# Performance work log

Measured on AMD Instinct MI355X. Metric: run time of the kernel, lower is better.

Reference implementation:

```python
import jax, jax.numpy as jnp
import numpy as np

N = 50000      # nodes
E = 800000     # edges
H = 128        # hidden_features
DEPTH = 5
G = 64         # graphs in batch
EPS = 1e-5


def _ln(x, g, b):
    m = jnp.mean(x, axis=-1, keepdims=True)
    v = jnp.mean((x - m) ** 2, axis=-1, keepdims=True)
    return (x - m) * jax.lax.rsqrt(v + EPS) * g + b


def _lin_init(key, fan_in, fan_out):
    s = 1.0 / np.sqrt(fan_in)
    kw, kb = jax.random.split(key)
    return (jax.random.uniform(kw, (fan_in, fan_out), jnp.float32, -s, s),
            jax.random.uniform(kb, (fan_out,), jnp.float32, -s, s))


def setup_inputs() -> dict:
    key = jax.random.key(0)
    ks = jax.random.split(key, 16)
    inp = {
        'x': jax.random.normal(ks[0], (N, 1), jnp.float32),
        'pos': jax.random.normal(ks[1], (N, 3), jnp.float32),
        'edge_index': jax.random.randint(ks[2], (2, E), 0, N, jnp.int32),
        'cell_offset': jax.random.normal(ks[3], (E, 3), jnp.float32),
        'unit_cell': jax.random.normal(ks[4], (3, 3), jnp.float32),
        'batch_ids': jnp.sort(jax.random.randint(ks[5], (N,), 0, G, jnp.int32)),
    }
    inp['emb_w'], inp['emb_b'] = _lin_init(ks[6], 1, H)
    # stacked per-layer params for lax.scan
    def stack(fn):
        outs = [fn(jax.random.fold_in(ks[7], i)) for i in range(DEPTH)]
        return tuple(jnp.stack(t) for t in zip(*outs))
    def layer_params(k):
        k1, k2, k3, k4 = jax.random.split(k, 4)
        mw1, mb1 = _lin_init(k1, 2 * H + 1, H)
        mw2, mb2 = _lin_init(k2, H, H)
        uw1, ub1 = _lin_init(k3, 2 * H, H)
        uw2, ub2 = _lin_init(k4, H, H)
        ones = jnp.ones((H,), jnp.float32); zeros = jnp.zeros((H,), jnp.float32)
        return (mw1, mb1, ones, zeros, mw2, mb2, ones, zeros,
                uw1, ub1, ones, zeros, uw2, ub2, ones, zeros)
    (inp['msg_w1'], inp['msg_b1'], inp['msg_g1'], inp['msg_be1'],
     inp['msg_w2'], inp['msg_b2'], inp['msg_g2'], inp['msg_be2'],
     inp['upd_w1'], inp['upd_b1'], inp['upd_g1'], inp['upd_be1'],
     inp['upd_w2'], inp['upd_b2'], inp['upd_g2'], inp['upd_be2']) = stack(layer_params)
    inp['pred_w1'], inp['pred_b1'] = _lin_init(ks[8], H, H)
    inp['pred_w2'], inp['pred_b2'] = _lin_init(ks[9], H, 1)
    return inp


def reference(x, pos, edge_index, cell_offset, unit_cell, batch_ids,
              emb_w, emb_b,
              msg_w1, msg_b1, msg_g1, msg_be1, msg_w2, msg_b2, msg_g2, msg_be2,
              upd_w1, upd_b1, upd_g1, upd_be1, upd_w2, upd_b2, upd_g2, upd_be2,
              pred_w1, pred_b1, pred_w2, pred_b2):
    src, dst = edge_index[0], edge_index[1]  # PyG: x_j = source, x_i = target
    h = x @ emb_w + emb_b  # [N, H]
    # PBC distances
    corrected = pos[dst] - cell_offset @ unit_cell  # [E, 3]
    dist = jnp.linalg.norm(corrected - pos[src], axis=-1, keepdims=True)  # [E, 1]

    def step(h, p):
        (mw1, mb1, mg1, mbe1, mw2, mb2, mg2, mbe2,
         uw1, ub1, ug1, ube1, uw2, ub2, ug2, ube2) = p
        msg = jnp.concatenate([h[dst], h[src], dist], axis=-1)  # [E, 2H+1]
        msg = jax.nn.relu(_ln(msg @ mw1 + mb1, mg1, mbe1))
        msg = jax.nn.relu(_ln(msg @ mw2 + mb2, mg2, mbe2))
        aggr = jax.ops.segment_sum(msg, dst, num_segments=N)  # scatter-add to targets
        u = jnp.concatenate([h, aggr], axis=-1)  # [N, 2H]
        u = jax.nn.relu(_ln(u @ uw1 + ub1, ug1, ube1))
        u = jax.nn.relu(_ln(u @ uw2 + ub2, ug2, ube2))
        return h + u, None  # residual

    params = (msg_w1, msg_b1, msg_g1, msg_be1, msg_w2, msg_b2, msg_g2, msg_be2,
              upd_w1, upd_b1, upd_g1, upd_be1, upd_w2, upd_b2, upd_g2, upd_be2)
    h, _ = jax.lax.scan(step, h, params)
    pooled = jax.ops.segment_sum(h, batch_ids, num_segments=G)  # global_add_pool
    return jax.nn.relu(pooled @ pred_w1 + pred_b1) @ pred_w2 + pred_b2  # [G, 1]
```

## Files before the change

kernel.cpp:

```cpp
#include <hip/hip_runtime.h>
#include <hip/hip_bf16.h>

#define NN 50000
#define NE 800000
#define HD 128
#define DEPTH 5
#define NG 64
#define LNEPS 1e-5f

typedef __attribute__((ext_vector_type(8))) short bf8;
typedef __attribute__((ext_vector_type(4))) float f4;

static __device__ __forceinline__ unsigned short bf1(float x) {
    __hip_bfloat16 b = __float2bfloat16(x);
    unsigned short r;
    __builtin_memcpy(&r, &b, 2);
    return r;
}
static __device__ __forceinline__ unsigned int cvt2(float a, float b) {
    float2 t; t.x = a; t.y = b;
    __hip_bfloat162 h = __float22bfloat162_rn(t);
    unsigned int r;
    __builtin_memcpy(&r, &h, 4);
    return r;
}


__global__ void pack_weights(const float* __restrict__ msg_w1, const float* __restrict__ msg_w2,
                             const float* __restrict__ upd_w1, const float* __restrict__ upd_w2,
                             unsigned short* __restrict__ packed) {
    const int which = blockIdx.y & 3, layer = blockIdx.y >> 2;
    const int t = blockIdx.x * 256 + threadIdx.x;
    unsigned short* lbase = packed + layer * 98304;
    if (which == 0) {
        if (t >= 32768) return;
        const int e = t & 7, l = (t >> 3) & 63, f = (t >> 9) & 15, s = t >> 13;
        const int k = s*32 + ((l >> 4) << 3) + e;
        const float* W = msg_w1 + layer*257*HD;
        const float v = (f < 8) ? W[k*HD + f*16 + (l & 15)]
                                : W[(k + 128)*HD + (f - 8)*16 + (l & 15)];
        lbase[t] = bf1(v);
        return;
    }
    const float* src; int K; unsigned short* dst;
    if (which == 1)      { src = msg_w2 + layer*HD*HD;  K = 128; dst = lbase + 32768; }
    else if (which == 2) { src = upd_w1 + layer*256*HD; K = 256; dst = lbase + 49152; }
    else                 { src = upd_w2 + layer*HD*HD;  K = 128; dst = lbase + 81920; }
    if (t >= K * HD) return;
    const int e = t & 7, l = (t >> 3) & 63, f = (t >> 9) & 7, s = t >> 12;
    const int kk = s*32 + ((l >> 4) << 3) + e;
    const int k = (which & 1) ? ((kk & 7)*16 + (kk >> 3)) : kk;
    const int n = f*16 + (l & 15);
    dst[t] = bf1(src[k*HD + n]);
}

__global__ void pack_sig(const float* __restrict__ msg_w1, const float* __restrict__ msg_g1,
                         const float* __restrict__ msg_be1, float* __restrict__ sig) {
    const int t = blockIdx.x * 256 + threadIdx.x;
    if (t >= DEPTH * 384) return;
    const int layer = t / 384, w3 = (t % 384) / 128, i = t % 128;
    const int col = (i & 7)*16 + (i >> 3);
    float v;
    if (w3 == 0)      v = msg_w1[layer*257*HD + 256*HD + col];
    else if (w3 == 1) v = msg_g1[layer*HD + col];
    else              v = msg_be1[layer*HD + col];
    sig[t] = v;
}

__global__ void embed_kernel(const float* __restrict__ x, const float* __restrict__ emb_w,
                             const float* __restrict__ emb_b,
                             float* __restrict__ h, unsigned short* __restrict__ hb) {
    const int i = blockIdx.x * 256 + threadIdx.x;
    const int n = i >> 7, j = i & 127;
    const float v = x[n] * emb_w[j] + emb_b[j];
    h[i] = v; hb[i] = bf1(v);
}

__global__ void hist_kernel(const int* __restrict__ ei, int* __restrict__ cnt) {
    const int e = blockIdx.x * 256 + threadIdx.x;
    atomicAdd(&cnt[ei[NE + e]], 1);
}

__global__ __launch_bounds__(1024) void scan_kernel(const int* __restrict__ cnt,
                                                    int* __restrict__ cur) {
    __shared__ int part[1024];
    const int t = threadIdx.x;
    const int per = 49;
    const int base = t * per;
    int s = 0;
    for (int i = 0; i < per; ++i) { const int idx = base + i; if (idx < NN) s += cnt[idx]; }
    part[t] = s; __syncthreads();
    for (int st = 1; st < 1024; st <<= 1) {
        const int v = (t >= st) ? part[t - st] : 0;
        __syncthreads();
        part[t] += v;
        __syncthreads();
    }
    int run = (t == 0) ? 0 : part[t - 1];
    for (int i = 0; i < per; ++i) {
        const int idx = base + i;
        if (idx < NN) { cur[idx] = run; run += cnt[idx]; }
    }
}

__global__ void scatter_kernel(const int* __restrict__ ei, int* __restrict__ cur,
                               int* __restrict__ sidx, int* __restrict__ ssrc,
                               int* __restrict__ sdst) {
    const int e = blockIdx.x * 256 + threadIdx.x;
    const int d = ei[NE + e];
    const int p = atomicAdd(&cur[d], 1);
    sidx[p] = e; ssrc[p] = ei[e]; sdst[p] = d;
}

__global__ void dist_kernel(const float* __restrict__ pos, const int* __restrict__ sidx,
                            const int* __restrict__ ssrc, const int* __restrict__ sdst,
                            const float* __restrict__ cell, const float* __restrict__ U,
                            float* __restrict__ dist) {
    const int p = blockIdx.x * 256 + threadIdx.x;
    const int e = sidx[p];
    const int s = ssrc[p], d = sdst[p];
    const float c0 = cell[e*3], c1 = cell[e*3+1], c2 = cell[e*3+2];
    const float ox = c0*U[0] + c1*U[3] + c2*U[6];
    const float oy = c0*U[1] + c1*U[4] + c2*U[7];
    const float oz = c0*U[2] + c1*U[5] + c2*U[8];
    const float dx = pos[d*3]   - ox - pos[s*3];
    const float dy = pos[d*3+1] - oy - pos[s*3+1];
    const float dz = pos[d*3+2] - oz - pos[s*3+2];
    dist[p] = sqrtf(dx*dx + dy*dy + dz*dz);
}

__global__ void y_kernel(const unsigned short* __restrict__ hb,
                         const unsigned short* __restrict__ pw,
                         const float* __restrict__ b1, unsigned short* __restrict__ y) {
    const int tid = threadIdx.x, blk = blockIdx.x;
    const int l = tid & 63, wv = tid >> 6;
    const int li = l & 15, gq = l >> 4;
    const int rowA = wv*32 + li, rowB = rowA + 16;
    const int nA = blk*64 + rowA, nB = blk*64 + rowB;
    const int ncA = (nA < NN) ? nA : NN - 1;
    const int ncB = (nB < NN) ? nB : NN - 1;
    const unsigned short* pHA = hb + ncA*HD + gq*8;
    const unsigned short* pHB = hb + ncB*HD + gq*8;

    f4 acc[2][16];
    #pragma unroll
    for (int m = 0; m < 2; ++m)
        #pragma unroll
        for (int f = 0; f < 16; ++f) { f4 z = {0.f,0.f,0.f,0.f}; acc[m][f] = z; }

    #pragma unroll
    for (int s = 0; s < 4; ++s) {
        const bf8 aA = *(const bf8*)(pHA + s*32);
        const bf8 aB = *(const bf8*)(pHB + s*32);
        #pragma unroll
        for (int f = 0; f < 16; ++f) {
            const bf8 b = *(const bf8*)(pw + s*8192 + f*512 + l*8);
            acc[0][f] = __builtin_amdgcn_mfma_f32_16x16x32_bf16(aA, b, acc[0][f], 0, 0, 0);
            acc[1][f] = __builtin_amdgcn_mfma_f32_16x16x32_bf16(aB, b, acc[1][f], 0, 0, 0);
        }
    }

    float bv[8];
    #pragma unroll
    for (int f = 0; f < 8; ++f) bv[f] = b1[f*16 + li];

    #pragma unroll
    for (int m = 0; m < 2; ++m)
        #pragma unroll
        for (int r = 0; r < 4; ++r) {
            const int node = blk*64 + wv*32 + m*16 + gq*4 + r;
            if (node < NN) {
                uint4 u;
                u.x = cvt2(acc[m][0][r]+bv[0], acc[m][1][r]+bv[1]);
                u.y = cvt2(acc[m][2][r]+bv[2], acc[m][3][r]+bv[3]);
                u.z = cvt2(acc[m][4][r]+bv[4], acc[m][5][r]+bv[5]);
                u.w = cvt2(acc[m][6][r]+bv[6], acc[m][7][r]+bv[7]);
                *(uint4*)(y + node*256 + li*8) = u;
                uint4 v;
                v.x = cvt2(acc[m][8][r],  acc[m][9][r]);
                v.y = cvt2(acc[m][10][r], acc[m][11][r]);
                v.z = cvt2(acc[m][12][r], acc[m][13][r]);
                v.w = cvt2(acc[m][14][r], acc[m][15][r]);
                *(uint4*)(y + node*256 + 128 + li*8) = v;
            }
        }
}

__global__ __launch_bounds__(128, 4) void edge_kernel(
    const unsigned short* __restrict__ y, const float* __restrict__ dist,
    const int* __restrict__ ssrc, const int* __restrict__ sdst,
    const unsigned short* __restrict__ pw2, const float* __restrict__ sig,
    const float* __restrict__ b2, const float* __restrict__ g2,
    const float* __restrict__ be2, float* __restrict__ aggr)
{
    __shared__ unsigned short lds[64 * 128];
    __shared__ int dstl[64];
    char* ldsb = (char*)lds;
    const int tid = threadIdx.x, blk = blockIdx.x;
    const int l = tid & 63, wv = tid >> 6;
    const int li = l & 15, gq = l >> 4;

    if (tid < 64) dstl[tid] = sdst[blk*64 + tid];

    {
        const int rl = l >> 1, half = l & 1;
        const int row = wv*32 + rl;
        const int e = blk*64 + row;
        const int dn = sdst[e], sn = ssrc[e];
        const float dv = dist[e];
        const unsigned short* pd = y + dn*256 + half*64;
        const unsigned short* pS = y + sn*256 + 128 + half*64;
        const float* wl = sig + half*64;

        float msum[64];
        #pragma unroll
        for (int c = 0; c < 8; ++c) {
            const uint4 ud = *(const uint4*)(pd + c*8);
            const uint4 us = *(const uint4*)(pS + c*8);
            const float4 wa = *(const float4*)(wl + c*8);
            const float4 wb = *(const float4*)(wl + c*8 + 4);
            const unsigned int du[4] = {ud.x, ud.y, ud.z, ud.w};
            const unsigned int su[4] = {us.x, us.y, us.z, us.w};
            const float ww[8] = {wa.x,wa.y,wa.z,wa.w, wb.x,wb.y,wb.z,wb.w};
            #pragma unroll
            for (int k = 0; k < 4; ++k) {
                const float d0 = __uint_as_float(du[k] << 16);
                const float d1 = __uint_as_float(du[k] & 0xffff0000u);
                const float s0 = __uint_as_float(su[k] << 16);
                const float s1 = __uint_as_float(su[k] & 0xffff0000u);
                msum[c*8 + 2*k]     = d0 + s0 + dv*ww[2*k];
                msum[c*8 + 2*k + 1] = d1 + s1 + dv*ww[2*k+1];
            }
        }
        float s1 = 0.f, s2 = 0.f;
        #pragma unroll
        for (int i = 0; i < 64; ++i) { s1 += msum[i]; s2 += msum[i]*msum[i]; }
        s1 += __shfl_xor(s1, 1);
        s2 += __shfl_xor(s2, 1);
        const float mean = s1 * (1.f/HD);
        const float rstd = rsqrtf(s2*(1.f/HD) - mean*mean + LNEPS);

        const float* g1p = sig + 128 + half*64;
        const float* e1p = sig + 256 + half*64;
        const int rsw = (row & 7) << 4;
        const int base = row*256 + half*128;
        #pragma unroll
        for (int c = 0; c < 8; ++c) {
            const float4 ga = *(const float4*)(g1p + c*8);
            const float4 gb = *(const float4*)(g1p + c*8 + 4);
            const float4 ea = *(const float4*)(e1p + c*8);
            const float4 eb = *(const float4*)(e1p + c*8 + 4);
            const float gg[8] = {ga.x,ga.y,ga.z,ga.w, gb.x,gb.y,gb.z,gb.w};
            const float ee[8] = {ea.x,ea.y,ea.z,ea.w, eb.x,eb.y,eb.z,eb.w};
            float t[8];
            #pragma unroll
            for (int k = 0; k < 8; ++k)
                t[k] = fmaxf((msum[c*8+k] - mean)*rstd*gg[k] + ee[k], 0.f);
            uint4 u;
            u.x = cvt2(t[0], t[1]); u.y = cvt2(t[2], t[3]);
            u.z = cvt2(t[4], t[5]); u.w = cvt2(t[6], t[7]);
            *(uint4*)(ldsb + ((base + c*16) ^ rsw)) = u;
        }
    }

    f4 acc2[2][8];
    #pragma unroll
    for (int m = 0; m < 2; ++m)
        #pragma unroll
        for (int f = 0; f < 8; ++f) { f4 z = {0.f,0.f,0.f,0.f}; acc2[m][f] = z; }
    #pragma unroll
    for (int s = 0; s < 4; ++s) {
        bf8 breg[8];
        #pragma unroll
        for (int f = 0; f < 8; ++f) breg[f] = *(const bf8*)(pw2 + s*4096 + f*512 + l*8);
        #pragma unroll
        for (int m = 0; m < 2; ++m) {
            const int ar = wv*32 + m*16 + li;
            const bf8 a = *(const bf8*)(ldsb + ((ar*256 + s*64 + gq*16) ^ ((ar & 7) << 4)));
            #pragma unroll
            for (int f = 0; f < 8; ++f)
                acc2[m][f] = __builtin_amdgcn_mfma_f32_16x16x32_bf16(a, breg[f], acc2[m][f], 0, 0, 0);
        }
    }

    {
        float bb2[8], gg2[8], be2v[8];
        #pragma unroll
        for (int f = 0; f < 8; ++f) {
            const int n = f*16 + li;
            bb2[f] = b2[n]; gg2[f] = g2[n]; be2v[f] = be2[n];
        }
        #pragma unroll
        for (int m = 0; m < 2; ++m) {
            float ps[4] = {0,0,0,0}, pq[4] = {0,0,0,0};
            #pragma unroll
            for (int f = 0; f < 8; ++f)
                #pragma unroll
                for (int r = 0; r < 4; ++r) {
                    const float v = acc2[m][f][r] + bb2[f];
                    acc2[m][f][r] = v;
                    ps[r] += v; pq[r] += v*v;
                }
            #pragma unroll
            for (int mm = 1; mm < 16; mm <<= 1)
                #pragma unroll
                for (int r = 0; r < 4; ++r) {
                    ps[r] += __shfl_xor(ps[r], mm);
                    pq[r] += __shfl_xor(pq[r], mm);
                }
            #pragma unroll
            for (int r = 0; r < 4; ++r) {
                const float mean = ps[r] * (1.f/HD);
                const float rstd = rsqrtf(pq[r]*(1.f/HD) - mean*mean + LNEPS);
                const int row = wv*32 + m*16 + gq*4 + r;
                float vv[8];
                #pragma unroll
                for (int f = 0; f < 8; ++f)
                    vv[f] = fmaxf((acc2[m][f][r] - mean)*rstd*gg2[f] + be2v[f], 0.f);
                uint4 u;
                u.x = cvt2(vv[0], vv[1]); u.y = cvt2(vv[2], vv[3]);
                u.z = cvt2(vv[4], vv[5]); u.w = cvt2(vv[6], vv[7]);
                *(uint4*)(ldsb + ((row*256 + li*16) ^ ((row & 7) << 4))) = u;
            }
        }
    }
    __syncthreads();

    {
        const int j = tid;
        const int jj = (j & 7)*16 + (j >> 3);
        int curd = dstl[0];
        float a0 = 0.f;
        #pragma unroll 4
        for (int row = 0; row < 64; ++row) {
            const int d = dstl[row];
            const unsigned short u = *(const unsigned short*)(ldsb + ((row*256 + j*2) ^ ((row & 7) << 4)));
            const float v = __uint_as_float(((unsigned int)u) << 16);
            if (d != curd) { unsafeAtomicAdd(&aggr[curd*HD + jj], a0); a0 = 0.f; curd = d; }
            a0 += v;
        }
        unsafeAtomicAdd(&aggr[curd*HD + jj], a0);
    }
}

__global__ __launch_bounds__(128, 4) void node_kernel(
    unsigned short* __restrict__ hb, float* __restrict__ aggr,
    const unsigned short* __restrict__ pw,
    const float* __restrict__ b1, const float* __restrict__ g1, const float* __restrict__ be1,
    const float* __restrict__ b2, const float* __restrict__ g2, const float* __restrict__ be2,
    float* __restrict__ h)
{
    __shared__ unsigned short lds[64 * 128];
    char* ldsb = (char*)lds;
    const int tid = threadIdx.x, blk = blockIdx.x;
    const int l = tid & 63, wv = tid >> 6;
    const int li = l & 15, gq = l >> 4;

    const int rowA = wv*32 + li, rowB = rowA + 16;
    const int nA = blk*64 + rowA, nB = blk*64 + rowB;
    const int ncA = (nA < NN) ? nA : NN - 1;
    const int ncB = (nB < NN) ? nB : NN - 1;
    const unsigned short* pHA = hb + ncA*HD + gq*8;
    const unsigned short* pHB = hb + ncB*HD + gq*8;
    float* pAA = aggr + ncA*HD + gq*8;
    float* pAB = aggr + ncB*HD + gq*8;

    f4 acc[2][8];
    #pragma unroll
    for (int m = 0; m < 2; ++m)
        #pragma unroll
        for (int f = 0; f < 8; ++f) { f4 z = {0.f,0.f,0.f,0.f}; acc[m][f] = z; }

    #pragma unroll
    for (int s = 0; s < 8; ++s) {
        bf8 breg[8];
        #pragma unroll
        for (int f = 0; f < 8; ++f) breg[f] = *(const bf8*)(pw + s*4096 + f*512 + l*8);
        bf8 aA, aB;
        if (s < 4) {
            aA = *(const bf8*)(pHA + s*32);
            aB = *(const bf8*)(pHB + s*32);
        } else {
            const float4 a0 = *(const float4*)(pAA + (s-4)*32);
            const float4 a1 = *(const float4*)(pAA + (s-4)*32 + 4);
            const float4 c0 = *(const float4*)(pAB + (s-4)*32);
            const float4 c1 = *(const float4*)(pAB + (s-4)*32 + 4);
            union { unsigned int u[4]; bf8 v; } pk;
            pk.u[0] = cvt2(a0.x, a0.y); pk.u[1] = cvt2(a0.z, a0.w);
            pk.u[2] = cvt2(a1.x, a1.y); pk.u[3] = cvt2(a1.z, a1.w);
            aA = pk.v;
            pk.u[0] = cvt2(c0.x, c0.y); pk.u[1] = cvt2(c0.z, c0.w);
            pk.u[2] = cvt2(c1.x, c1.y); pk.u[3] = cvt2(c1.z, c1.w);
            aB = pk.v;
        }
        #pragma unroll
        for (int f = 0; f < 8; ++f) {
            acc[0][f] = __builtin_amdgcn_mfma_f32_16x16x32_bf16(aA, breg[f], acc[0][f], 0, 0, 0);
            acc[1][f] = __builtin_amdgcn_mfma_f32_16x16x32_bf16(aB, breg[f], acc[1][f], 0, 0, 0);
        }
    }

    {
        const float4 z = {0.f,0.f,0.f,0.f};
        #pragma unroll
        for (int s = 0; s < 4; ++s) {
            if (nA < NN) { *(float4*)(pAA + s*32) = z; *(float4*)(pAA + s*32 + 4) = z; }
            if (nB < NN) { *(float4*)(pAB + s*32) = z; *(float4*)(pAB + s*32 + 4) = z; }
        }
    }

    {
        float bb[8], gg[8], be[8];
        #pragma unroll
        for (int f = 0; f < 8; ++f) {
            const int n = f*16 + li;
            bb[f] = b1[n]; gg[f] = g1[n]; be[f] = be1[n];
        }
        #pragma unroll
        for (int m = 0; m < 2; ++m) {
            float ps[4] = {0,0,0,0}, pq[4] = {0,0,0,0};
            #pragma unroll
            for (int f = 0; f < 8; ++f)
                #pragma unroll
                for (int r = 0; r < 4; ++r) {
                    const float v = acc[m][f][r] + bb[f];
                    acc[m][f][r] = v;
                    ps[r] += v; pq[r] += v*v;
                }
            #pragma unroll
            for (int mm = 1; mm < 16; mm <<= 1)
                #pragma unroll
                for (int r = 0; r < 4; ++r) {
                    ps[r] += __shfl_xor(ps[r], mm);
                    pq[r] += __shfl_xor(pq[r], mm);
                }
            #pragma unroll
            for (int r = 0; r < 4; ++r) {
                const float mean = ps[r] * (1.f/HD);
                const float rstd = rsqrtf(pq[r]*(1.f/HD) - mean*mean + LNEPS);
                const int row = wv*32 + m*16 + gq*4 + r;
                float vv[8];
                #pragma unroll
                for (int f = 0; f < 8; ++f)
                    vv[f] = fmaxf((acc[m][f][r] - mean)*rstd*gg[f] + be[f], 0.f);
                uint4 u;
                u.x = cvt2(vv[0], vv[1]); u.y = cvt2(vv[2], vv[3]);
                u.z = cvt2(vv[4], vv[5]); u.w = cvt2(vv[6], vv[7]);
                *(uint4*)(ldsb + ((row*256 + li*16) ^ ((row & 7) << 4))) = u;
            }
        }
    }

    const unsigned short* pw2 = pw + 32768;
    f4 acc2[2][8];
    #pragma unroll
    for (int m = 0; m < 2; ++m)
        #pragma unroll
        for (int f = 0; f < 8; ++f) { f4 z = {0.f,0.f,0.f,0.f}; acc2[m][f] = z; }
    #pragma unroll
    for (int s = 0; s < 4; ++s) {
        bf8 breg[8];
        #pragma unroll
        for (int f = 0; f < 8; ++f) breg[f] = *(const bf8*)(pw2 + s*4096 + f*512 + l*8);
        #pragma unroll
        for (int m = 0; m < 2; ++m) {
            const int ar = wv*32 + m*16 + li;
            const bf8 a = *(const bf8*)(ldsb + ((ar*256 + s*64 + gq*16) ^ ((ar & 7) << 4)));
            #pragma unroll
            for (int f = 0; f < 8; ++f)
                acc2[m][f] = __builtin_amdgcn_mfma_f32_16x16x32_bf16(a, breg[f], acc2[m][f], 0, 0, 0);
        }
    }

    {
        float bb2[8], gg2[8], be2v[8];
        #pragma unroll
        for (int f = 0; f < 8; ++f) {
            const int n = f*16 + li;
            bb2[f] = b2[n]; gg2[f] = g2[n]; be2v[f] = be2[n];
        }
        #pragma unroll
        for (int m = 0; m < 2; ++m) {
            float ps[4] = {0,0,0,0}, pq[4] = {0,0,0,0};
            #pragma unroll
            for (int f = 0; f < 8; ++f)
                #pragma unroll
                for (int r = 0; r < 4; ++r) {
                    const float v = acc2[m][f][r] + bb2[f];
                    acc2[m][f][r] = v;
                    ps[r] += v; pq[r] += v*v;
                }
            #pragma unroll
            for (int mm = 1; mm < 16; mm <<= 1)
                #pragma unroll
                for (int r = 0; r < 4; ++r) {
                    ps[r] += __shfl_xor(ps[r], mm);
                    pq[r] += __shfl_xor(pq[r], mm);
                }
            #pragma unroll
            for (int r = 0; r < 4; ++r) {
                const int node = blk*64 + wv*32 + m*16 + gq*4 + r;
                if (node < NN) {
                    const float mean = ps[r] * (1.f/HD);
                    const float rstd = rsqrtf(pq[r]*(1.f/HD) - mean*mean + LNEPS);
                    #pragma unroll
                    for (int f = 0; f < 8; ++f) {
                        const int n = f*16 + li;
                        float v = (acc2[m][f][r] - mean)*rstd*gg2[f] + be2v[f];
                        v = fmaxf(v, 0.f);
                        const int idx = node*HD + n;
                        const float nh = h[idx] + v;
                        h[idx] = nh;
                        hb[idx] = bf1(nh);
                    }
                }
            }
        }
    }
}

__global__ void pool_kernel(const float* __restrict__ h, const int* __restrict__ bids,
                            float* __restrict__ pooled) {
    const int j = threadIdx.x;
    const int n0 = blockIdx.x * 256;
    if (n0 >= NN) return;
    int cur = bids[n0];
    float acc = 0.f;
    for (int i = 0; i < 256; ++i) {
        const int n = n0 + i;
        if (n >= NN) break;
        const int b = bids[n];
        if (b != cur) { unsafeAtomicAdd(&pooled[cur*HD + j], acc); acc = 0.f; cur = b; }
        acc += h[n*HD + j];
    }
    unsafeAtomicAdd(&pooled[cur*HD + j], acc);
}

__global__ void pred_kernel(const float* __restrict__ pooled, const float* __restrict__ w1,
                            const float* __restrict__ pb1, const float* __restrict__ w2,
                            const float* __restrict__ pb2, float* __restrict__ out) {
    const int g = blockIdx.x, j = threadIdx.x;
    __shared__ float pg[128];
    __shared__ float red[128];
    pg[j] = pooled[g*HD + j];
    __syncthreads();
    float z = pb1[j];
    for (int k = 0; k < 128; ++k) z += pg[k] * w1[k*HD + j];
    red[j] = fmaxf(z, 0.f) * w2[j];
    __syncthreads();
    for (int st = 64; st > 0; st >>= 1) {
        if (j < st) red[j] += red[j + st];
        __syncthreads();
    }
    if (j == 0) out[g] = red[0] + pb2[0];
}

extern "C" void kernel_launch(void* const* d_in, const int* in_sizes, int n_in,
                              void* d_out, int out_size, void* d_ws, size_t ws_size,
                              hipStream_t stream) {
    const float* x       = (const float*)d_in[0];
    const float* pos     = (const float*)d_in[1];
    const int*   ei      = (const int*)  d_in[2];
    const float* cell    = (const float*)d_in[3];
    const float* U       = (const float*)d_in[4];
    const int*   bids    = (const int*)  d_in[5];
    const float* emb_w   = (const float*)d_in[6];
    const float* emb_b   = (const float*)d_in[7];
    const float* msg_w1  = (const float*)d_in[8];
    const float* msg_b1  = (const float*)d_in[9];
    const float* msg_g1  = (const float*)d_in[10];
    const float* msg_be1 = (const float*)d_in[11];
    const float* msg_w2  = (const float*)d_in[12];
    const float* msg_b2  = (const float*)d_in[13];
    const float* msg_g2  = (const float*)d_in[14];
    const float* msg_be2 = (const float*)d_in[15];
    const float* upd_w1  = (const float*)d_in[16];
    const float* upd_b1  = (const float*)d_in[17];
    const float* upd_g1  = (const float*)d_in[18];
    const float* upd_be1 = (const float*)d_in[19];
    const float* upd_w2  = (const float*)d_in[20];
    const float* upd_b2  = (const float*)d_in[21];
    const float* upd_g2  = (const float*)d_in[22];
    const float* upd_be2 = (const float*)d_in[23];
    const float* pred_w1 = (const float*)d_in[24];
    const float* pred_b1 = (const float*)d_in[25];
    const float* pred_w2 = (const float*)d_in[26];
    const float* pred_b2 = (const float*)d_in[27];

    char* ws = (char*)d_ws;
    float*          h      = (float*)          ws;
    unsigned short* hb     = (unsigned short*)(ws + 25600000);
    float*          aggr   = (float*)         (ws + 38400000);
    float*          dist   = (float*)         (ws + 64000000);
    float*          pooled = (float*)         (ws + 67200000);
    unsigned short* packed = (unsigned short*)(ws + 67232768);
    int*            cnt    = (int*)           (ws + 68215808);
    int*            cur    = (int*)           (ws + 68416512);
    int*            sidx   = (int*)           (ws + 68617216);
    int*            ssrc   = (int*)           (ws + 71817216);
    int*            sdst   = (int*)           (ws + 75017216);
    float*          sig    = (float*)         (ws + 78217216);
    unsigned short* y      = (unsigned short*)(ws + 78224896);

    hipMemsetAsync(aggr, 0, (size_t)NN * HD * sizeof(float), stream);
    hipMemsetAsync(pooled, 0, (size_t)NG * HD * sizeof(float), stream);
    hipMemsetAsync(cnt, 0, (size_t)NN * sizeof(int), stream);

    dim3 pgrid(128, DEPTH * 4);
    pack_weights<<<pgrid, 256, 0, stream>>>(msg_w1, msg_w2, upd_w1, upd_w2, packed);
    pack_sig<<<(DEPTH*384 + 255)/256, 256, 0, stream>>>(msg_w1, msg_g1, msg_be1, sig);
    embed_kernel<<<(NN * HD) / 256, 256, 0, stream>>>(x, emb_w, emb_b, h, hb);

    hist_kernel<<<NE / 256, 256, 0, stream>>>(ei, cnt);
    scan_kernel<<<1, 1024, 0, stream>>>(cnt, cur);
    scatter_kernel<<<NE / 256, 256, 0, stream>>>(ei, cur, sidx, ssrc, sdst);
    dist_kernel<<<NE / 256, 256, 0, stream>>>(pos, sidx, ssrc, sdst, cell, U, dist);

    for (int layer = 0; layer < DEPTH; ++layer) {
        const unsigned short* pl = packed + layer * 98304;
        y_kernel<<<(NN + 63) / 64, 128, 0, stream>>>(hb, pl, msg_b1 + layer*HD, y);
        edge_kernel<<<NE / 64, 128, 0, stream>>>(
            y, dist, ssrc, sdst, pl + 32768, sig + layer*384,
            msg_b2 + layer*HD, msg_g2 + layer*HD, msg_be2 + layer*HD,
            aggr);
        node_kernel<<<(NN + 63) / 64, 128, 0, stream>>>(
            hb, aggr, pl + 49152,
            upd_b1 + layer*HD, upd_g1 + layer*HD, upd_be1 + layer*HD,
            upd_b2 + layer*HD, upd_g2 + layer*HD, upd_be2 + layer*HD,
            h);
    }

    pool_kernel<<<(NN + 255) / 256, 128, 0, stream>>>(h, bids, pooled);
    pred_kernel<<<NG, 128, 0, stream>>>(pooled, pred_w1, pred_b1, pred_w2, pred_b2, (float*)d_out);
}
```

Before: 1.494 ms.

## Use four waves per block in node kernels, widen LDS swizzle, pair-column edge scatter

New measurement: 1.509 ms. No clear change (+1.0%).

```diff
diff --git a/kernel.cpp b/kernel.cpp
--- a/kernel.cpp
+++ b/kernel.cpp
@@ -129,34 +129,28 @@
     dist[p] = sqrtf(dx*dx + dy*dy + dz*dz);
 }
 
-__global__ void y_kernel(const unsigned short* __restrict__ hb,
+__global__ __launch_bounds__(256, 4) void y_kernel(const unsigned short* __restrict__ hb,
                          const unsigned short* __restrict__ pw,
                          const float* __restrict__ b1, unsigned short* __restrict__ y) {
     const int tid = threadIdx.x, blk = blockIdx.x;
     const int l = tid & 63, wv = tid >> 6;
     const int li = l & 15, gq = l >> 4;
-    const int rowA = wv*32 + li, rowB = rowA + 16;
-    const int nA = blk*64 + rowA, nB = blk*64 + rowB;
-    const int ncA = (nA < NN) ? nA : NN - 1;
-    const int ncB = (nB < NN) ? nB : NN - 1;
-    const unsigned short* pHA = hb + ncA*HD + gq*8;
-    const unsigned short* pHB = hb + ncB*HD + gq*8;
-
-    f4 acc[2][16];
-    #pragma unroll
-    for (int m = 0; m < 2; ++m)
-        #pragma unroll
-        for (int f = 0; f < 16; ++f) { f4 z = {0.f,0.f,0.f,0.f}; acc[m][f] = z; }
+    const int row = wv*16 + li;
+    const int node0 = blk*64 + row;
+    const int nc = (node0 < NN) ? node0 : NN - 1;
+    const unsigned short* pH = hb + nc*HD + gq*8;
+
+    f4 acc[16];
+    #pragma unroll
+    for (int f = 0; f < 16; ++f) { f4 z = {0.f,0.f,0.f,0.f}; acc[f] = z; }
 
     #pragma unroll
     for (int s = 0; s < 4; ++s) {
-        const bf8 aA = *(const bf8*)(pHA + s*32);
-        const bf8 aB = *(const bf8*)(pHB + s*32);
+        const bf8 a = *(const bf8*)(pH + s*32);
         #pragma unroll
         for (int f = 0; f < 16; ++f) {
             const bf8 b = *(const bf8*)(pw + s*8192 + f*512 + l*8);
-            acc[0][f] = __builtin_amdgcn_mfma_f32_16x16x32_bf16(aA, b, acc[0][f], 0, 0, 0);
-            acc[1][f] = __builtin_amdgcn_mfma_f32_16x16x32_bf16(aB, b, acc[1][f], 0, 0, 0);
+            acc[f] = __builtin_amdgcn_mfma_f32_16x16x32_bf16(a, b, acc[f], 0, 0, 0);
         }
     }
 
@@ -165,25 +159,23 @@
     for (int f = 0; f < 8; ++f) bv[f] = b1[f*16 + li];
 
     #pragma unroll
-    for (int m = 0; m < 2; ++m)
-        #pragma unroll
-        for (int r = 0; r < 4; ++r) {
-            const int node = blk*64 + wv*32 + m*16 + gq*4 + r;
-            if (node < NN) {
-                uint4 u;
-                u.x = cvt2(acc[m][0][r]+bv[0], acc[m][1][r]+bv[1]);
-                u.y = cvt2(acc[m][2][r]+bv[2], acc[m][3][r]+bv[3]);
-                u.z = cvt2(acc[m][4][r]+bv[4], acc[m][5][r]+bv[5]);
-                u.w = cvt2(acc[m][6][r]+bv[6], acc[m][7][r]+bv[7]);
-                *(uint4*)(y + node*256 + li*8) = u;
-                uint4 v;
-                v.x = cvt2(acc[m][8][r],  acc[m][9][r]);
-                v.y = cvt2(acc[m][10][r], acc[m][11][r]);
-                v.z = cvt2(acc[m][12][r], acc[m][13][r]);
-                v.w = cvt2(acc[m][14][r], acc[m][15][r]);
-                *(uint4*)(y + node*256 + 128 + li*8) = v;
-            }
-        }
+    for (int r = 0; r < 4; ++r) {
+        const int node = blk*64 + wv*16 + gq*4 + r;
+        if (node < NN) {
+            uint4 u;
+            u.x = cvt2(acc[0][r]+bv[0], acc[1][r]+bv[1]);
+            u.y = cvt2(acc[2][r]+bv[2], acc[3][r]+bv[3]);
+            u.z = cvt2(acc[4][r]+bv[4], acc[5][r]+bv[5]);
+            u.w = cvt2(acc[6][r]+bv[6], acc[7][r]+bv[7]);
+            *(uint4*)(y + node*256 + li*8) = u;
+            uint4 v;
+            v.x = cvt2(acc[8][r],  acc[9][r]);
+            v.y = cvt2(acc[10][r], acc[11][r]);
+            v.z = cvt2(acc[12][r], acc[13][r]);
+            v.w = cvt2(acc[14][r], acc[15][r]);
+            *(uint4*)(y + node*256 + 128 + li*8) = v;
+        }
+    }
 }
 
 __global__ __launch_bounds__(128, 4) void edge_kernel(
@@ -242,7 +234,7 @@
 
         const float* g1p = sig + 128 + half*64;
         const float* e1p = sig + 256 + half*64;
-        const int rsw = (row & 7) << 4;
+        const int rsw = (row & 15) << 4;
         const int base = row*256 + half*128;
         #pragma unroll
         for (int c = 0; c < 8; ++c) {
@@ -276,7 +268,7 @@
         #pragma unroll
         for (int m = 0; m < 2; ++m) {
             const int ar = wv*32 + m*16 + li;
-            const bf8 a = *(const bf8*)(ldsb + ((ar*256 + s*64 + gq*16) ^ ((ar & 7) << 4)));
+            const bf8 a = *(const bf8*)(ldsb + ((ar*256 + s*64 + gq*16) ^ ((ar & 15) << 4)));
             #pragma unroll
             for (int f = 0; f < 8; ++f)
                 acc2[m][f] = __builtin_amdgcn_mfma_f32_16x16x32_bf16(a, breg[f], acc2[m][f], 0, 0, 0);
@@ -320,30 +312,39 @@
                 uint4 u;
                 u.x = cvt2(vv[0], vv[1]); u.y = cvt2(vv[2], vv[3]);
                 u.z = cvt2(vv[4], vv[5]); u.w = cvt2(vv[6], vv[7]);
-                *(uint4*)(ldsb + ((row*256 + li*16) ^ ((row & 7) << 4))) = u;
+                *(uint4*)(ldsb + ((row*256 + li*16) ^ ((row & 15) << 4))) = u;
             }
         }
     }
     __syncthreads();
 
     {
-        const int j = tid;
-        const int jj = (j & 7)*16 + (j >> 3);
-        int curd = dstl[0];
-        float a0 = 0.f;
+        const int jp = tid & 63, hh = tid >> 6;
+        const int j0 = jp*2, j1 = j0 + 1;
+        const int jj0 = (j0 & 7)*16 + (j0 >> 3);
+        const int jj1 = (j1 & 7)*16 + (j1 >> 3);
+        const int r0 = hh * 32;
+        int curd = dstl[r0];
+        float a0 = 0.f, a1 = 0.f;
         #pragma unroll 4
-        for (int row = 0; row < 64; ++row) {
+        for (int i = 0; i < 32; ++i) {
+            const int row = r0 + i;
             const int d = dstl[row];
-            const unsigned short u = *(const unsigned short*)(ldsb + ((row*256 + j*2) ^ ((row & 7) << 4)));
-            const float v = __uint_as_float(((unsigned int)u) << 16);
-            if (d != curd) { unsafeAtomicAdd(&aggr[curd*HD + jj], a0); a0 = 0.f; curd = d; }
-            a0 += v;
-        }
-        unsafeAtomicAdd(&aggr[curd*HD + jj], a0);
-    }
-}
-
-__global__ __launch_bounds__(128, 4) void node_kernel(
+            const unsigned int u = *(const unsigned int*)(ldsb + ((row*256 + jp*4) ^ ((row & 15) << 4)));
+            if (d != curd) {
+                unsafeAtomicAdd(&aggr[curd*HD + jj0], a0);
+                unsafeAtomicAdd(&aggr[curd*HD + jj1], a1);
+                a0 = a1 = 0.f; curd = d;
+            }
+            a0 += __uint_as_float(u << 16);
+            a1 += __uint_as_float(u & 0xffff0000u);
+        }
+        unsafeAtomicAdd(&aggr[curd*HD + jj0], a0);
+        unsafeAtomicAdd(&aggr[curd*HD + jj1], a1);
+    }
+}
+
+__global__ __launch_bounds__(256, 4) void node_kernel(
     unsigned short* __restrict__ hb, float* __restrict__ aggr,
     const unsigned short* __restrict__ pw,
     const float* __restrict__ b1, const float* __restrict__ g1, const float* __restrict__ be1,
@@ -356,56 +357,42 @@
     const int l = tid & 63, wv = tid >> 6;
     const int li = l & 15, gq = l >> 4;
 
-    const int rowA = wv*32 + li, rowB = rowA + 16;
-    const int nA = blk*64 + rowA, nB = blk*64 + rowB;
-    const int ncA = (nA < NN) ? nA : NN - 1;
-    const int ncB = (nB < NN) ? nB : NN - 1;
-    const unsigned short* pHA = hb + ncA*HD + gq*8;
-    const unsigned short* pHB = hb + ncB*HD + gq*8;
-    float* pAA = aggr + ncA*HD + gq*8;
-    float* pAB = aggr + ncB*HD + gq*8;
-
-    f4 acc[2][8];
-    #pragma unroll
-    for (int m = 0; m < 2; ++m)
-        #pragma unroll
-        for (int f = 0; f < 8; ++f) { f4 z = {0.f,0.f,0.f,0.f}; acc[m][f] = z; }
+    const int row = wv*16 + li;
+    const int nA = blk*64 + row;
+    const int nc = (nA < NN) ? nA : NN - 1;
+    const unsigned short* pH = hb + nc*HD + gq*8;
+    float* pA = aggr + nc*HD + gq*8;
+
+    f4 acc[8];
+    #pragma unroll
+    for (int f = 0; f < 8; ++f) { f4 z = {0.f,0.f,0.f,0.f}; acc[f] = z; }
 
     #pragma unroll
     for (int s = 0; s < 8; ++s) {
         bf8 breg[8];
         #pragma unroll
         for (int f = 0; f < 8; ++f) breg[f] = *(const bf8*)(pw + s*4096 + f*512 + l*8);
-        bf8 aA, aB;
+        bf8 a;
         if (s < 4) {
-            aA = *(const bf8*)(pHA + s*32);
-            aB = *(const bf8*)(pHB + s*32);
+            a = *(const bf8*)(pH + s*32);
         } else {
-            const float4 a0 = *(const float4*)(pAA + (s-4)*32);
-            const float4 a1 = *(const float4*)(pAA + (s-4)*32 + 4);
-            const float4 c0 = *(const float4*)(pAB + (s-4)*32);
-            const float4 c1 = *(const float4*)(pAB + (s-4)*32 + 4);
+            const float4 a0 = *(const float4*)(pA + (s-4)*32);
+            const float4 a1 = *(const float4*)(pA + (s-4)*32 + 4);
             union { unsigned int u[4]; bf8 v; } pk;
             pk.u[0] = cvt2(a0.x, a0.y); pk.u[1] = cvt2(a0.z, a0.w);
             pk.u[2] = cvt2(a1.x, a1.y); pk.u[3] = cvt2(a1.z, a1.w);
-            aA = pk.v;
-            pk.u[0] = cvt2(c0.x, c0.y); pk.u[1] = cvt2(c0.z, c0.w);
-            pk.u[2] = cvt2(c1.x, c1.y); pk.u[3] = cvt2(c1.z, c1.w);
-            aB = pk.v;
-        }
-        #pragma unroll
-        for (int f = 0; f < 8; ++f) {
-            acc[0][f] = __builtin_amdgcn_mfma_f32_16x16x32_bf16(aA, breg[f], acc[0][f], 0, 0, 0);
-            acc[1][f] = __builtin_amdgcn_mfma_f32_16x16x32_bf16(aB, breg[f], acc[1][f], 0, 0, 0);
-        }
+            a = pk.v;
+        }
+        #pragma unroll
+        for (int f = 0; f < 8; ++f)
+            acc[f] = __builtin_amdgcn_mfma_f32_16x16x32_bf16(a, breg[f], acc[f], 0, 0, 0);
     }
 
     {
         const float4 z = {0.f,0.f,0.f,0.f};
-        #pragma unroll
-        for (int s = 0; s < 4; ++s) {
-            if (nA < NN) { *(float4*)(pAA + s*32) = z; *(float4*)(pAA + s*32 + 4) = z; }
-            if (nB < NN) { *(float4*)(pAB + s*32) = z; *(float4*)(pAB + s*32 + 4) = z; }
+        if (nA < NN) {
+            #pragma unroll
+            for (int s = 0; s < 4; ++s) { *(float4*)(pA + s*32) = z; *(float4*)(pA + s*32 + 4) = z; }
         }
     }
 
@@ -416,60 +403,52 @@
             const int n = f*16 + li;
             bb[f] = b1[n]; gg[f] = g1[n]; be[f] = be1[n];
         }
-        #pragma unroll
-        for (int m = 0; m < 2; ++m) {
-            float ps[4] = {0,0,0,0}, pq[4] = {0,0,0,0};
+        float ps[4] = {0,0,0,0}, pq[4] = {0,0,0,0};
+        #pragma unroll
+        for (int f = 0; f < 8; ++f)
+            #pragma unroll
+            for (int r = 0; r < 4; ++r) {
+                const float v = acc[f][r] + bb[f];
+                acc[f][r] = v;
+                ps[r] += v; pq[r] += v*v;
+            }
+        #pragma unroll
+        for (int mm = 1; mm < 16; mm <<= 1)
+            #pragma unroll
+            for (int r = 0; r < 4; ++r) {
+                ps[r] += __shfl_xor(ps[r], mm);
+                pq[r] += __shfl_xor(pq[r], mm);
+            }
+        #pragma unroll
+        for (int r = 0; r < 4; ++r) {
+            const float mean = ps[r] * (1.f/HD);
+            const float rstd = rsqrtf(pq[r]*(1.f/HD) - mean*mean + LNEPS);
+            const int rw = wv*16 + gq*4 + r;
+            float vv[8];
             #pragma unroll
             for (int f = 0; f < 8; ++f)
-                #pragma unroll
-                for (int r = 0; r < 4; ++r) {
-                    const float v = acc[m][f][r] + bb[f];
-                    acc[m][f][r] = v;
-                    ps[r] += v; pq[r] += v*v;
-                }
-            #pragma unroll
-            for (int mm = 1; mm < 16; mm <<= 1)
-                #pragma unroll
-                for (int r = 0; r < 4; ++r) {
-                    ps[r] += __shfl_xor(ps[r], mm);
-                    pq[r] += __shfl_xor(pq[r], mm);
-                }
-            #pragma unroll
-            for (int r = 0; r < 4; ++r) {
-                const float mean = ps[r] * (1.f/HD);
-                const float rstd = rsqrtf(pq[r]*(1.f/HD) - mean*mean + LNEPS);
-                const int row = wv*32 + m*16 + gq*4 + r;
-                float vv[8];
-                #pragma unroll
-                for (int f = 0; f < 8; ++f)
-                    vv[f] = fmaxf((acc[m][f][r] - mean)*rstd*gg[f] + be[f], 0.f);
-                uint4 u;
-                u.x = cvt2(vv[0], vv[1]); u.y = cvt2(vv[2], vv[3]);
-                u.z = cvt2(vv[4], vv[5]); u.w = cvt2(vv[6], vv[7]);
-                *(uint4*)(ldsb + ((row*256 + li*16) ^ ((row & 7) << 4))) = u;
-            }
+                vv[f] = fmaxf((acc[f][r] - mean)*rstd*gg[f] + be[f], 0.f);
+            uint4 u;
+            u.x = cvt2(vv[0], vv[1]); u.y = cvt2(vv[2], vv[3]);
+            u.z = cvt2(vv[4], vv[5]); u.w = cvt2(vv[6], vv[7]);
+            *(uint4*)(ldsb + ((rw*256 + li*16) ^ ((rw & 15) << 4))) = u;
         }
     }
 
     const unsigned short* pw2 = pw + 32768;
-    f4 acc2[2][8];
-    #pragma unroll
-    for (int m = 0; m < 2; ++m)
-        #pragma unroll
-        for (int f = 0; f < 8; ++f) { f4 z = {0.f,0.f,0.f,0.f}; acc2[m][f] = z; }
+    f4 acc2[8];
+    #pragma unroll
+    for (int f = 0; f < 8; ++f) { f4 z = {0.f,0.f,0.f,0.f}; acc2[f] = z; }
     #pragma unroll
     for (int s = 0; s < 4; ++s) {
         bf8 breg[8];
         #pragma unroll
         for (int f = 0; f < 8; ++f) breg[f] = *(const bf8*)(pw2 + s*4096 + f*512 + l*8);
-        #pragma unroll
-        for (int m = 0; m < 2; ++m) {
-            const int ar = wv*32 + m*16 + li;
-            const bf8 a = *(const bf8*)(ldsb + ((ar*256 + s*64 + gq*16) ^ ((ar & 7) << 4)));
-            #pragma unroll
-            for (int f = 0; f < 8; ++f)
-                acc2[m][f] = __builtin_amdgcn_mfma_f32_16x16x32_bf16(a, breg[f], acc2[m][f], 0, 0, 0);
-        }
+        const int ar = wv*16 + li;
+        const bf8 a = *(const bf8*)(ldsb + ((ar*256 + s*64 + gq*16) ^ ((ar & 15) << 4)));
+        #pragma unroll
+        for (int f = 0; f < 8; ++f)
+            acc2[f] = __builtin_amdgcn_mfma_f32_16x16x32_bf16(a, breg[f], acc2[f], 0, 0, 0);
     }
 
     {
@@ -479,40 +458,37 @@
             const int n = f*16 + li;
             bb2[f] = b2[n]; gg2[f] = g2[n]; be2v[f] = be2[n];
         }
-        #pragma unroll
-        for (int m = 0; m < 2; ++m) {
-            float ps[4] = {0,0,0,0}, pq[4] = {0,0,0,0};
-            #pragma unroll
-            for (int f = 0; f < 8; ++f)
+        float ps[4] = {0,0,0,0}, pq[4] = {0,0,0,0};
+        #pragma unroll
+        for (int f = 0; f < 8; ++f)
+            #pragma unroll
+            for (int r = 0; r < 4; ++r) {
+                const float v = acc2[f][r] + bb2[f];
+                acc2[f][r] = v;
+                ps[r] += v; pq[r] += v*v;
+            }
+        #pragma unroll
+        for (int mm = 1; mm < 16; mm <<= 1)
+            #pragma unroll
+            for (int r = 0; r < 4; ++r) {
+                ps[r] += __shfl_xor(ps[r], mm);
+                pq[r] += __shfl_xor(pq[r], mm);
+            }
+        #pragma unroll
+        for (int r = 0; r < 4; ++r) {
+            const int node = blk*64 + wv*16 + gq*4 + r;
+            if (node < NN) {
+                const float mean = ps[r] * (1.f/HD);
+                const float rstd = rsqrtf(pq[r]*(1.f/HD) - mean*mean + LNEPS);
                 #pragma unroll
-                for (int r = 0; r < 4; ++r) {
-                    const float v = acc2[m][f][r] + bb2[f];
-                    acc2[m][f][r] = v;
-                    ps[r] += v; pq[r] += v*v;
-                }
-            #pragma unroll
-            for (int mm = 1; mm < 16; mm <<= 1)
-                #pragma unroll
-                for (int r = 0; r < 4; ++r) {
-                    ps[r] += __shfl_xor(ps[r], mm);
-                    pq[r] += __shfl_xor(pq[r], mm);
-                }
-            #pragma unroll
-            for (int r = 0; r < 4; ++r) {
-                const int node = blk*64 + wv*32 + m*16 + gq*4 + r;
-                if (node < NN) {
-                    const float mean = ps[r] * (1.f/HD);
-                    const float rstd = rsqrtf(pq[r]*(1.f/HD) - mean*mean + LNEPS);
-                    #pragma unroll
-                    for (int f = 0; f < 8; ++f) {
-                        const int n = f*16 + li;
-                        float v = (acc2[m][f][r] - mean)*rstd*gg2[f] + be2v[f];
-                        v = fmaxf(v, 0.f);
-                        const int idx = node*HD + n;
-                        const float nh = h[idx] + v;
-                        h[idx] = nh;
-                        hb[idx] = bf1(nh);
-                    }
+                for (int f = 0; f < 8; ++f) {
+                    const int n = f*16 + li;
+                    float v = (acc2[f][r] - mean)*rstd*gg2[f] + be2v[f];
+                    v = fmaxf(v, 0.f);
+                    const int idx = node*HD + n;
+                    const float nh = h[idx] + v;
+                    h[idx] = nh;
+                    hb[idx] = bf1(nh);
                 }
             }
         }
@@ -618,12 +594,12 @@
 
     for (int layer = 0; layer < DEPTH; ++layer) {
         const unsigned short* pl = packed + layer * 98304;
-        y_kernel<<<(NN + 63) / 64, 128, 0, stream>>>(hb, pl, msg_b1 + layer*HD, y);
+        y_kernel<<<(NN + 63) / 64, 256, 0, stream>>>(hb, pl, msg_b1 + layer*HD, y);
         edge_kernel<<<NE / 64, 128, 0, stream>>>(
             y, dist, ssrc, sdst, pl + 32768, sig + layer*384,
             msg_b2 + layer*HD, msg_g2 + layer*HD, msg_be2 + layer*HD,
             aggr);
-        node_kernel<<<(NN + 63) / 64, 128, 0, stream>>>(
+        node_kernel<<<(NN + 63) / 64, 256, 0, stream>>>(
             hb, aggr, pl + 49152,
             upd_b1 + layer*HD, upd_g1 + layer*HD, upd_be1 + layer*HD,
             upd_b2 + layer*HD, upd_g2 + layer*HD, upd_be2 + layer*HD,
```
